# Kernel tuning notes

Hardware: AMD Instinct MI355X
Metric: run time of the kernel (lower is better)

## Reference

```python
import jax, jax.numpy as jnp
import numpy as np

B, NUM_CAMS, C, N_ANCHOR = 1, 6, 256, 900
NUM_LEVELS, NUM_FIXED, NUM_LEARN, NUM_GROUPS = 4, 7, 6, 8
NUM_PTS = NUM_FIXED + NUM_LEARN
IMG_W, IMG_H = 704, 256
SHAPES = [(64, 176), (32, 88), (16, 44), (8, 22)]  # strides 4,8,16,32


def setup_inputs() -> dict:
    key = jax.random.key(0)
    ks = jax.random.split(key, 12)
    sum_hw = sum(h * w for h, w in SHAPES)
    feature = jax.random.normal(ks[0], (B, NUM_CAMS, sum_hw, C), jnp.float32)
    spatial_shapes = jnp.array(SHAPES, dtype=jnp.int32)
    starts = np.cumsum([0] + [h * w for h, w in SHAPES[:-1]])
    level_start_index = jnp.array(starts, dtype=jnp.int32)
    # anchor: [x,y,z, log(w),log(l),log(h), sin(yaw), cos(yaw), vx,vy,vz]
    center = jax.random.uniform(ks[1], (B, N_ANCHOR, 3), minval=-40.0, maxval=40.0) * jnp.array([1.0, 1.0, 0.05])
    size = jnp.log(jnp.array([2.0, 4.5, 1.7])) * jnp.ones((B, N_ANCHOR, 3))
    yaw = jax.random.uniform(ks[2], (B, N_ANCHOR, 1), minval=-np.pi, maxval=np.pi)
    anchor = jnp.concatenate([center, size, jnp.sin(yaw), jnp.cos(yaw), jnp.zeros((B, N_ANCHOR, 3))], axis=-1).astype(jnp.float32)
    instance_feature = jax.random.normal(ks[3], (B, N_ANCHOR, C), jnp.float32)
    time_interval = jnp.full((B,), 0.5, jnp.float32)
    # plausible lidar2img = K @ [R|t] for 6 surround cameras
    l2i = []
    for c in range(NUM_CAMS):
        a = 2.0 * np.pi * c / NUM_CAMS
        Rz = np.array([[np.cos(a), -np.sin(a), 0.0], [np.sin(a), np.cos(a), 0.0], [0.0, 0.0, 1.0]])
        swap = np.array([[0.0, -1.0, 0.0], [0.0, 0.0, -1.0], [1.0, 0.0, 0.0]])  # lidar axes -> camera axes
        Rcam = swap @ Rz.T
        t = -Rcam @ np.array([0.0, 0.0, 1.5])
        E = np.eye(4); E[:3, :3] = Rcam; E[:3, 3] = t
        K = np.eye(4); K[0, 0] = K[1, 1] = 400.0; K[0, 2] = IMG_W / 2.0; K[1, 2] = IMG_H / 2.0
        l2i.append(K @ E)
    lidar2img = jnp.asarray(np.broadcast_to(np.stack(l2i)[None], (B, NUM_CAMS, 4, 4)), jnp.float32)
    image_wh = jnp.broadcast_to(jnp.array([IMG_W, IMG_H], jnp.float32), (B, NUM_CAMS, 2))
    s = 0.02
    n_w = NUM_CAMS * NUM_LEVELS * NUM_PTS * NUM_GROUPS
    return dict(
        instance_feature=instance_feature, anchor=anchor, time_interval=time_interval,
        feature=feature, spatial_shapes=spatial_shapes, level_start_index=level_start_index,
        lidar2img=lidar2img, image_wh=image_wh,
        enc_w=jax.random.normal(ks[4], (11, C)) * s, enc_b=jnp.zeros((C,), jnp.float32),
        kp_fixed=jax.random.normal(ks[5], (NUM_FIXED, 3)) * 0.5,
        kp_w=jax.random.normal(ks[6], (C, NUM_LEARN * 3)) * s, kp_b=jnp.zeros((NUM_LEARN * 3,), jnp.float32),
        wfc_w=jax.random.normal(ks[7], (C, n_w)) * s, wfc_b=jnp.zeros((n_w,), jnp.float32),
        out_w=jax.random.normal(ks[8], (C, C)) * s, out_b=jnp.zeros((C,), jnp.float32),
    )


def _bilinear_sample(feature, spatial_shapes, level_start_index, pts, valid):
    # feature: [B,Cm,sumHW,C]; pts: [B,Cm,N,P,2] normalized to [0,1]; valid: [B,Cm,N,P]
    Bn, Cm, _, Cd = feature.shape
    N, P = pts.shape[2], pts.shape[3]
    per_level = []
    for l in range(NUM_LEVELS):
        H = spatial_shapes[l, 0]
        W = spatial_shapes[l, 1]
        start = level_start_index[l]
        # grid_sample align_corners=False convention
        x = pts[..., 0] * W - 0.5
        y = pts[..., 1] * H - 0.5
        x0f = jnp.floor(x); y0f = jnp.floor(y)
        wx = (x - x0f)[..., None]
        wy = (y - y0f)[..., None]
        x0 = x0f.astype(jnp.int32); y0 = y0f.astype(jnp.int32)

        def gather(xi, yi):
            ok = (xi >= 0) & (xi < W) & (yi >= 0) & (yi < H) & valid
            xi_c = jnp.clip(xi, 0, W - 1)
            yi_c = jnp.clip(yi, 0, H - 1)
            idx = (start + yi_c * W + xi_c).reshape(Bn, Cm, N * P, 1)
            g = jnp.take_along_axis(feature, idx, axis=2).reshape(Bn, Cm, N, P, Cd)
            return g * ok[..., None]

        v = (gather(x0, y0) * (1 - wx) * (1 - wy)
             + gather(x0 + 1, y0) * wx * (1 - wy)
             + gather(x0, y0 + 1) * (1 - wx) * wy
             + gather(x0 + 1, y0 + 1) * wx * wy)
        per_level.append(v)
    return jnp.stack(per_level, axis=4)  # [B,Cm,N,P,L,C]


def _forward(instance_feature, anchor, feature, spatial_shapes, level_start_index,
             lidar2img, image_wh, enc_w, enc_b, kp_fixed, kp_w, kp_b, wfc_w, wfc_b, out_w, out_b):
    Bn, N, Cd = instance_feature.shape
    anchor_embed = anchor @ enc_w + enc_b                      # anchor_encoder
    # --- keypoint generation (7 fixed + 6 learnable), scaled by box size, rotated by yaw ---
    center = anchor[..., :3]
    size = jnp.exp(anchor[..., 3:6])
    sin_y, cos_y = anchor[..., 6:7], anchor[..., 7:8]
    learn = (instance_feature @ kp_w + kp_b).reshape(Bn, N, NUM_LEARN, 3)
    offs = jnp.concatenate([jnp.broadcast_to(kp_fixed, (Bn, N, NUM_FIXED, 3)), learn], axis=2)
    offs = offs * size[:, :, None, :]
    ox, oy, oz = offs[..., 0], offs[..., 1], offs[..., 2]
    rx = cos_y * ox - sin_y * oy
    ry = sin_y * ox + cos_y * oy
    kp = jnp.stack([rx, ry, oz], axis=-1) + center[:, :, None, :]          # [B,N,P,3]
    # --- project to each camera ---
    kp_h = jnp.concatenate([kp, jnp.ones_like(kp[..., :1])], axis=-1)
    p = jnp.einsum('bcij,bnpj->bcnpi', lidar2img, kp_h)                    # [B,Cm,N,P,4]
    depth = p[..., 2]
    xy = p[..., :2] / jnp.clip(depth, 1e-5, None)[..., None]
    pts = xy / image_wh[:, :, None, None, :]                               # [0,1] normalized
    valid = depth > 1e-5
    # --- multi-scale multi-camera bilinear gather ---
    feats = _bilinear_sample(feature, spatial_shapes, level_start_index, pts, valid)  # [B,Cm,N,P,L,C]
    # --- group-wise attention weights, softmax over cams*levels*pts ---
    w = ((instance_feature + anchor_embed) @ wfc_w + wfc_b).reshape(Bn, N, -1, NUM_GROUPS)
    w = jax.nn.softmax(w, axis=-2).reshape(Bn, N, NUM_CAMS, NUM_LEVELS, NUM_PTS, NUM_GROUPS)
    f = jnp.transpose(feats, (0, 2, 1, 4, 3, 5)).reshape(
        Bn, N, NUM_CAMS, NUM_LEVELS, NUM_PTS, NUM_GROUPS, Cd // NUM_GROUPS)
    agg = jnp.sum(f * w[..., None], axis=(2, 3, 4)).reshape(Bn, N, Cd)
    return instance_feature + (agg @ out_w + out_b)


def reference(instance_feature, anchor, time_interval, feature, spatial_shapes, level_start_index,
              lidar2img, image_wh, enc_w, enc_b, kp_fixed, kp_w, kp_b, wfc_w, wfc_b, out_w, out_b):
    # time_interval is only consumed by the 'refine' op, which is not in the executed op list
    return _forward(instance_feature, anchor, feature, spatial_shapes, level_start_index,
                    lidar2img, image_wh, enc_w, enc_b, kp_fixed, kp_w, kp_b, wfc_w, wfc_b, out_w, out_b)
```

## Files before the change

### kernel.cpp

```cpp
#include <hip/hip_runtime.h>
#include <math.h>

#define N_ANCHOR   900
#define NUM_CAMS   6
#define CDIM       256
#define NUM_LEVELS 4
#define NUM_FIXED  7
#define NUM_LEARN  6
#define NUM_PTS    13
#define NUM_GROUPS 8
#define NW         2496
#define NI         312
#define SUM_HW     14960

typedef short short8 __attribute__((ext_vector_type(8)));
typedef float floatx4 __attribute__((ext_vector_type(4)));

__device__ __forceinline__ unsigned short f2bf(float x) {
  unsigned u = __float_as_uint(x);
  u += 0x7FFFu + ((u >> 16) & 1u);
  return (unsigned short)(u >> 16);
}

__global__ __launch_bounds__(256) void k_prep(
    const float* __restrict__ inst, const float* __restrict__ anchor,
    const float* __restrict__ l2i, const float* __restrict__ image_wh,
    const float* __restrict__ kp_fixed, const float* __restrict__ kp_w,
    const float* __restrict__ kp_b,
    const float* __restrict__ enc_w, const float* __restrict__ enc_b,
    unsigned short* __restrict__ qbf, float* __restrict__ pts_out,
    float* __restrict__ valid_out) {
  const int n = blockIdx.x;
  const int t = threadIdx.x;
  __shared__ float anc[11];
  __shared__ float learn[NUM_LEARN * 3];
  __shared__ float kps[NUM_PTS][3];
  __shared__ float ins[CDIM];

  const float iv = inst[n * CDIM + t];
  ins[t] = iv;
  if (t < 11) anc[t] = anchor[n * 11 + t];
  __syncthreads();

  {
    float s = enc_b[t] + iv;
    #pragma unroll
    for (int k = 0; k < 11; ++k) s += anc[k] * enc_w[k * CDIM + t];
    qbf[n * CDIM + t] = f2bf(s);
  }

  if (t < NUM_LEARN * 3) {
    float s = kp_b[t];
    for (int k = 0; k < CDIM; ++k) s += ins[k] * kp_w[k * (NUM_LEARN * 3) + t];
    learn[t] = s;
  }
  __syncthreads();

  if (t < NUM_PTS) {
    const float sx = expf(anc[3]), sy = expf(anc[4]), sz = expf(anc[5]);
    float ox, oy, oz;
    if (t < NUM_FIXED) {
      ox = kp_fixed[t * 3 + 0]; oy = kp_fixed[t * 3 + 1]; oz = kp_fixed[t * 3 + 2];
    } else {
      const int j = (t - NUM_FIXED) * 3;
      ox = learn[j + 0]; oy = learn[j + 1]; oz = learn[j + 2];
    }
    ox *= sx; oy *= sy; oz *= sz;
    const float sn = anc[6], cs = anc[7];
    kps[t][0] = cs * ox - sn * oy + anc[0];
    kps[t][1] = sn * ox + cs * oy + anc[1];
    kps[t][2] = oz + anc[2];
  }
  __syncthreads();

  if (t < NUM_CAMS * NUM_PTS) {
    const int cam = t / NUM_PTS, p = t % NUM_PTS;
    const float* M = l2i + cam * 16;
    const float kx = kps[p][0], ky = kps[p][1], kz = kps[p][2];
    const float px = M[0] * kx + M[1] * ky + M[2]  * kz + M[3];
    const float py = M[4] * kx + M[5] * ky + M[6]  * kz + M[7];
    const float pz = M[8] * kx + M[9] * ky + M[10] * kz + M[11];
    const float d = fmaxf(pz, 1e-5f);
    const float u = (px / d) / image_wh[cam * 2 + 0];
    const float v = (py / d) / image_wh[cam * 2 + 1];
    const int o = n * NUM_CAMS * NUM_PTS + t;
    pts_out[o * 2 + 0] = u;
    pts_out[o * 2 + 1] = v;
    valid_out[o] = (pz > 1e-5f) ? 1.0f : 0.0f;
  }
}

__global__ __launch_bounds__(256) void k_cvtw(
    const float* __restrict__ wfc_w, unsigned short* __restrict__ wbf_t) {
  const int n0 = blockIdx.x * 64, k0 = blockIdx.y * 64;
  const int t = threadIdx.x;
  __shared__ float tile[64][65];
  #pragma unroll
  for (int i = 0; i < 4; ++i) {
    const int kr = (t >> 4) + i * 16;
    const int nc = (t & 15) * 4;
    const float4 v = *(const float4*)&wfc_w[(size_t)(k0 + kr) * NW + n0 + nc];
    tile[kr][nc + 0] = v.x; tile[kr][nc + 1] = v.y;
    tile[kr][nc + 2] = v.z; tile[kr][nc + 3] = v.w;
  }
  __syncthreads();
  #pragma unroll
  for (int i = 0; i < 4; ++i) {
    const int nr = (t >> 4) + i * 16;
    const int kc = (t & 15) * 4;
    ushort4 o;
    o.x = f2bf(tile[kc + 0][nr]);
    o.y = f2bf(tile[kc + 1][nr]);
    o.z = f2bf(tile[kc + 2][nr]);
    o.w = f2bf(tile[kc + 3][nr]);
    *(ushort4*)&wbf_t[(size_t)(n0 + nr) * CDIM + k0 + kc] = o;
  }
}

__global__ __launch_bounds__(256) void k_wgemm(
    const unsigned short* __restrict__ qbf,
    const unsigned short* __restrict__ wbf_t,
    const float* __restrict__ wfc_b, float* __restrict__ raw) {
  const int tid = threadIdx.x;
  const int w = tid >> 6;
  const int l = tid & 63;
  const int n0 = blockIdx.x * 64;
  const int m0 = blockIdx.y * 64;
  __shared__ unsigned short Bs[64 * 64];

  floatx4 acc[4];
  #pragma unroll
  for (int s = 0; s < 4; ++s) acc[s] = (floatx4){0.f, 0.f, 0.f, 0.f};

  const int arow = m0 + w * 16 + (l & 15);
  const bool arow_ok = arow < N_ANCHOR;
  const unsigned short* aptr = qbf + (size_t)arow * CDIM + (l >> 4) * 8;

  for (int k0 = 0; k0 < CDIM; k0 += 64) {
    #pragma unroll
    for (int i = 0; i < 2; ++i) {
      const int idx = tid + i * 256;
      const int n = idx >> 3, kg = idx & 7;
      const short8 bv =
          *(const short8*)&wbf_t[(size_t)(n0 + n) * CDIM + k0 + kg * 8];
      *(short8*)&Bs[n * 64 + ((kg ^ (n & 7)) * 8)] = bv;
    }
    __syncthreads();
    #pragma unroll
    for (int c = 0; c < 2; ++c) {
      short8 a = (short8){0, 0, 0, 0, 0, 0, 0, 0};
      if (arow_ok) a = *(const short8*)&aptr[k0 + c * 32];
      #pragma unroll
      for (int s = 0; s < 4; ++s) {
        const int nloc = s * 16 + (l & 15);
        const int k8 = c * 4 + (l >> 4);
        const short8 b = *(const short8*)&Bs[nloc * 64 + ((k8 ^ (nloc & 7)) * 8)];
        acc[s] = __builtin_amdgcn_mfma_f32_16x16x32_bf16(a, b, acc[s], 0, 0, 0);
      }
    }
    __syncthreads();
  }

  const int colb = n0 + (l & 15);
  const int rowb = m0 + w * 16 + (l >> 4) * 4;
  #pragma unroll
  for (int s = 0; s < 4; ++s) {
    const int col = colb + s * 16;
    const float bias = wfc_b[col];
    #pragma unroll
    for (int r = 0; r < 4; ++r) {
      const int row = rowb + r;
      if (row < N_ANCHOR)
        raw[(size_t)row * NW + col] = acc[s][r] + bias;
    }
  }
}

__global__ __launch_bounds__(256) void k_smstats(
    const float* __restrict__ raw, float* __restrict__ stats) {
  const int n = blockIdx.x, t = threadIdx.x;
  __shared__ float row_s[NW];
  const float4* src = (const float4*)(raw + (size_t)n * NW);
  for (int j = t; j < NW / 4; j += 256)
    *(float4*)&row_s[j * 4] = src[j];
  __syncthreads();
  const int g = t >> 5, lane = t & 31;
  float m = -1e30f;
  for (int i = lane; i < NI; i += 32) m = fmaxf(m, row_s[i * NUM_GROUPS + g]);
  #pragma unroll
  for (int o = 16; o > 0; o >>= 1) m = fmaxf(m, __shfl_down(m, o, 32));
  m = __shfl(m, 0, 32);
  float s = 0.0f;
  for (int i = lane; i < NI; i += 32) s += expf(row_s[i * NUM_GROUPS + g] - m);
  #pragma unroll
  for (int o = 16; o > 0; o >>= 1) s += __shfl_down(s, o, 32);
  if (lane == 0) {
    stats[n * 16 + g] = m;
    stats[n * 16 + 8 + g] = 1.0f / s;
  }
}

__global__ __launch_bounds__(256) void k_sample(
    const float* __restrict__ feature,
    const int* __restrict__ spatial_shapes, const int* __restrict__ level_start,
    const float* __restrict__ pts, const float* __restrict__ valid,
    const float* __restrict__ raw, const float* __restrict__ stats,
    float* __restrict__ agg) {
  const int n = blockIdx.x;
  const int cam = blockIdx.y;
  const int t = threadIdx.x;
  const int q = t >> 6;
  const int ci = t & 63;
  const int g = ci >> 3;
  __shared__ float w_s[NUM_LEVELS * NUM_PTS * NUM_GROUPS];
  __shared__ float uv_s[NUM_PTS][2];
  __shared__ float val_s[NUM_PTS];
  __shared__ float mx_s[NUM_GROUPS], inv_s[NUM_GROUPS];
  __shared__ int shp[NUM_LEVELS][2];
  __shared__ int lst[NUM_LEVELS];
  __shared__ int any_valid;
  __shared__ float4 red[256];

  if (t < NUM_PTS) {
    const int o = (n * NUM_CAMS + cam) * NUM_PTS + t;
    uv_s[t][0] = pts[o * 2 + 0];
    uv_s[t][1] = pts[o * 2 + 1];
    val_s[t] = valid[o];
  }
  if (t < NUM_GROUPS) {
    mx_s[t]  = stats[n * 16 + t];
    inv_s[t] = stats[n * 16 + 8 + t];
  }
  if (t < NUM_LEVELS) {
    shp[t][0] = spatial_shapes[t * 2 + 0];
    shp[t][1] = spatial_shapes[t * 2 + 1];
    lst[t] = level_start[t];
  }
  if (t == 0) any_valid = 0;
  __syncthreads();
  if (t < NUM_PTS && val_s[t] != 0.0f) any_valid = 1;
  __syncthreads();

  float* aout = agg + ((size_t)n * NUM_CAMS + cam) * CDIM;
  if (!any_valid) {
    if (t < 64) *(float4*)&aout[t * 4] = make_float4(0.f, 0.f, 0.f, 0.f);
    return;
  }

  for (int j = t; j < 416; j += 256)
    w_s[j] = expf(raw[(size_t)n * NW + cam * 416 + j] - mx_s[j & 7]) * inv_s[j & 7];
  __syncthreads();

  const int dx = q & 1, dy = q >> 1;
  float4 acc = make_float4(0.f, 0.f, 0.f, 0.f);
  const float* fcam = feature + (size_t)cam * SUM_HW * CDIM;
  for (int p = 0; p < NUM_PTS; ++p) {
    if (val_s[p] == 0.0f) continue;
    const float u = uv_s[p][0], v = uv_s[p][1];
    #pragma unroll
    for (int l = 0; l < NUM_LEVELS; ++l) {
      const int H = shp[l][0], W = shp[l][1], st = lst[l];
      const float x = u * (float)W - 0.5f;
      const float y = v * (float)H - 0.5f;
      const float x0f = floorf(x), y0f = floorf(y);
      const float wx = x - x0f, wy = y - y0f;
      const int xx = (int)x0f + dx;
      const int yy = (int)y0f + dy;
      if (xx >= 0 && xx < W && yy >= 0 && yy < H) {
        const float cw = w_s[(l * NUM_PTS + p) * 8 + g]
                       * (dx ? wx : 1.0f - wx) * (dy ? wy : 1.0f - wy);
        const float4 f = *(const float4*)&fcam[(size_t)(st + yy * W + xx) * CDIM + ci * 4];
        acc.x += cw * f.x; acc.y += cw * f.y;
        acc.z += cw * f.z; acc.w += cw * f.w;
      }
    }
  }
  red[t] = acc;
  __syncthreads();
  if (t < 64) {
    float4 s = red[t];
    const float4 b1 = red[t + 64], b2 = red[t + 128], b3 = red[t + 192];
    s.x += b1.x + b2.x + b3.x;
    s.y += b1.y + b2.y + b3.y;
    s.z += b1.z + b2.z + b3.z;
    s.w += b1.w + b2.w + b3.w;
    *(float4*)&aout[t * 4] = s;
  }
}

__global__ __launch_bounds__(1024) void k_out(
    const float* __restrict__ inst, const float* __restrict__ agg,
    const float* __restrict__ out_w, const float* __restrict__ out_b,
    float* __restrict__ out) {
  const int n = blockIdx.x, t = threadIdx.x;
  const int col = t & 255, ks = t >> 8;
  __shared__ float a_s[CDIM];
  __shared__ float red[4][CDIM];

  if (t < CDIM) {
    float s = 0.0f;
    #pragma unroll
    for (int cam = 0; cam < NUM_CAMS; ++cam)
      s += agg[((size_t)n * NUM_CAMS + cam) * CDIM + t];
    a_s[t] = s;
  }
  __syncthreads();

  float partial = 0.0f;
  const int k0 = ks * 64;
  #pragma unroll
  for (int k = 0; k < 64; ++k)
    partial += a_s[k0 + k] * out_w[(k0 + k) * CDIM + col];
  red[ks][col] = partial;
  __syncthreads();

  if (t < CDIM) {
    const float s = red[0][t] + red[1][t] + red[2][t] + red[3][t];
    out[(size_t)n * CDIM + t] = s + out_b[t] + inst[(size_t)n * CDIM + t];
  }
}

extern "C" void kernel_launch(void* const* d_in, const int* in_sizes, int n_in,
                              void* d_out, int out_size, void* d_ws, size_t ws_size,
                              hipStream_t stream) {
  const float* inst           = (const float*)d_in[0];
  const float* anchor         = (const float*)d_in[1];
  const float* feature        = (const float*)d_in[3];
  const int*   spatial_shapes = (const int*)d_in[4];
  const int*   level_start    = (const int*)d_in[5];
  const float* l2i            = (const float*)d_in[6];
  const float* image_wh       = (const float*)d_in[7];
  const float* enc_w          = (const float*)d_in[8];
  const float* enc_b          = (const float*)d_in[9];
  const float* kp_fixed       = (const float*)d_in[10];
  const float* kp_w           = (const float*)d_in[11];
  const float* kp_b           = (const float*)d_in[12];
  const float* wfc_w          = (const float*)d_in[13];
  const float* wfc_b          = (const float*)d_in[14];
  const float* out_w          = (const float*)d_in[15];
  const float* out_b          = (const float*)d_in[16];

  float* ws    = (float*)d_ws;
  float* pts   = ws;
  float* valid = pts + N_ANCHOR * NUM_CAMS * NUM_PTS * 2;
  float* wbuf  = valid + N_ANCHOR * NUM_CAMS * NUM_PTS;
  float* stats = wbuf + (size_t)N_ANCHOR * NW;
  float* agg   = stats + N_ANCHOR * 16;
  unsigned short* qbf   = (unsigned short*)(agg + N_ANCHOR * NUM_CAMS * CDIM);
  unsigned short* wbf_t = qbf + N_ANCHOR * CDIM;

  k_prep<<<N_ANCHOR, 256, 0, stream>>>(inst, anchor, l2i, image_wh,
                                       kp_fixed, kp_w, kp_b, enc_w, enc_b,
                                       qbf, pts, valid);
  k_cvtw<<<dim3(NW / 64, CDIM / 64), 256, 0, stream>>>(wfc_w, wbf_t);
  k_wgemm<<<dim3(NW / 64, (N_ANCHOR + 63) / 64), 256, 0, stream>>>(
      qbf, wbf_t, wfc_b, wbuf);
  k_smstats<<<N_ANCHOR, 256, 0, stream>>>(wbuf, stats);
  k_sample<<<dim3(N_ANCHOR, NUM_CAMS), 256, 0, stream>>>(
      feature, spatial_shapes, level_start, pts, valid, wbuf, stats, agg);
  k_out<<<N_ANCHOR, 1024, 0, stream>>>(inst, agg, out_w, out_b, (float*)d_out);
}
```

Before: 233.1 us.

## Compact valid sample taps via ballot and batch output GEMM over two anchors

In the sampling kernel, each wave now computes all 52 point-level tap offsets and bilinear coefficients in parallel. It compacts the in-bounds taps with a ballot/popcount into shared lists and then runs a branch-free loop unrolled by four over them. This removes per-tap divergent bounds checks and lets several independent feature loads be in flight at once. The output projection kernel now handles two anchors per block so each out_w load is reused twice, which halves weight traffic and the block count.

```diff
diff --git a/kernel.cpp b/kernel.cpp
--- a/kernel.cpp
+++ b/kernel.cpp
@@ -210,8 +210,8 @@
   const int cam = blockIdx.y;
   const int t = threadIdx.x;
   const int q = t >> 6;
-  const int ci = t & 63;
-  const int g = ci >> 3;
+  const int lane = t & 63;
+  const int g = lane >> 3;
   __shared__ float w_s[NUM_LEVELS * NUM_PTS * NUM_GROUPS];
   __shared__ float uv_s[NUM_PTS][2];
   __shared__ float val_s[NUM_PTS];
@@ -219,6 +219,9 @@
   __shared__ int shp[NUM_LEVELS][2];
   __shared__ int lst[NUM_LEVELS];
   __shared__ int any_valid;
+  __shared__ int   joff[4][56];
+  __shared__ float jcf[4][56];
+  __shared__ int   jw[4][56];
   __shared__ float4 red[256];
 
   if (t < NUM_PTS) {
@@ -249,30 +252,54 @@
 
   for (int j = t; j < 416; j += 256)
     w_s[j] = expf(raw[(size_t)n * NW + cam * 416 + j] - mx_s[j & 7]) * inv_s[j & 7];
-  __syncthreads();
-
-  const int dx = q & 1, dy = q >> 1;
-  float4 acc = make_float4(0.f, 0.f, 0.f, 0.f);
-  const float* fcam = feature + (size_t)cam * SUM_HW * CDIM;
-  for (int p = 0; p < NUM_PTS; ++p) {
-    if (val_s[p] == 0.0f) continue;
-    const float u = uv_s[p][0], v = uv_s[p][1];
-    #pragma unroll
-    for (int l = 0; l < NUM_LEVELS; ++l) {
+
+  bool ok = false;
+  int off = 0, wb = 0;
+  float cf = 0.0f;
+  if (lane < 52) {
+    const int p = lane >> 2, l = lane & 3;
+    if (val_s[p] != 0.0f) {
       const int H = shp[l][0], W = shp[l][1], st = lst[l];
-      const float x = u * (float)W - 0.5f;
-      const float y = v * (float)H - 0.5f;
+      const float x = uv_s[p][0] * (float)W - 0.5f;
+      const float y = uv_s[p][1] * (float)H - 0.5f;
       const float x0f = floorf(x), y0f = floorf(y);
       const float wx = x - x0f, wy = y - y0f;
+      const int dx = q & 1, dy = q >> 1;
       const int xx = (int)x0f + dx;
       const int yy = (int)y0f + dy;
       if (xx >= 0 && xx < W && yy >= 0 && yy < H) {
-        const float cw = w_s[(l * NUM_PTS + p) * 8 + g]
-                       * (dx ? wx : 1.0f - wx) * (dy ? wy : 1.0f - wy);
-        const float4 f = *(const float4*)&fcam[(size_t)(st + yy * W + xx) * CDIM + ci * 4];
-        acc.x += cw * f.x; acc.y += cw * f.y;
-        acc.z += cw * f.z; acc.w += cw * f.w;
+        ok = true;
+        off = (st + yy * W + xx) * CDIM;
+        cf = (dx ? wx : 1.0f - wx) * (dy ? wy : 1.0f - wy);
+        wb = (l * NUM_PTS + p) * 8;
       }
+    }
+  }
+  const unsigned long long mask = __ballot(ok);
+  const int nj = __popcll(mask);
+  if (ok) {
+    const int pos = __popcll(mask & ((1ull << lane) - 1ull));
+    joff[q][pos] = off;
+    jcf[q][pos] = cf;
+    jw[q][pos] = wb;
+  }
+  const int padded = (nj + 3) & ~3;
+  if (lane >= nj && lane < padded) {
+    joff[q][lane] = 0; jcf[q][lane] = 0.0f; jw[q][lane] = 0;
+  }
+  __syncthreads();
+
+  float4 acc = make_float4(0.f, 0.f, 0.f, 0.f);
+  const float* fcam = feature + (size_t)cam * SUM_HW * CDIM;
+  const int cio = lane * 4;
+  for (int j = 0; j < padded; j += 4) {
+    #pragma unroll
+    for (int i = 0; i < 4; ++i) {
+      const int o = joff[q][j + i];
+      const float wgt = jcf[q][j + i] * w_s[jw[q][j + i] + g];
+      const float4 f = *(const float4*)&fcam[o + cio];
+      acc.x += wgt * f.x; acc.y += wgt * f.y;
+      acc.z += wgt * f.z; acc.w += wgt * f.w;
     }
   }
   red[t] = acc;
@@ -292,31 +319,37 @@
     const float* __restrict__ inst, const float* __restrict__ agg,
     const float* __restrict__ out_w, const float* __restrict__ out_b,
     float* __restrict__ out) {
-  const int n = blockIdx.x, t = threadIdx.x;
+  const int n0 = blockIdx.x * 2, t = threadIdx.x;
   const int col = t & 255, ks = t >> 8;
-  __shared__ float a_s[CDIM];
-  __shared__ float red[4][CDIM];
-
-  if (t < CDIM) {
+  __shared__ float a_s[2][CDIM];
+  __shared__ float red[4][2][CDIM];
+
+  if (t < 512) {
+    const int a = t >> 8, c = t & 255;
     float s = 0.0f;
     #pragma unroll
     for (int cam = 0; cam < NUM_CAMS; ++cam)
-      s += agg[((size_t)n * NUM_CAMS + cam) * CDIM + t];
-    a_s[t] = s;
-  }
-  __syncthreads();
-
-  float partial = 0.0f;
+      s += agg[((size_t)(n0 + a) * NUM_CAMS + cam) * CDIM + c];
+    a_s[a][c] = s;
+  }
+  __syncthreads();
+
+  float p0 = 0.0f, p1 = 0.0f;
   const int k0 = ks * 64;
   #pragma unroll
-  for (int k = 0; k < 64; ++k)
-    partial += a_s[k0 + k] * out_w[(k0 + k) * CDIM + col];
-  red[ks][col] = partial;
-  __syncthreads();
-
-  if (t < CDIM) {
-    const float s = red[0][t] + red[1][t] + red[2][t] + red[3][t];
-    out[(size_t)n * CDIM + t] = s + out_b[t] + inst[(size_t)n * CDIM + t];
+  for (int k = 0; k < 64; ++k) {
+    const float w = out_w[(k0 + k) * CDIM + col];
+    p0 += a_s[0][k0 + k] * w;
+    p1 += a_s[1][k0 + k] * w;
+  }
+  red[ks][0][col] = p0;
+  red[ks][1][col] = p1;
+  __syncthreads();
+
+  if (t < 512) {
+    const int a = t >> 8, c = t & 255;
+    const float s = red[0][a][c] + red[1][a][c] + red[2][a][c] + red[3][a][c];
+    out[(size_t)(n0 + a) * CDIM + c] = s + out_b[c] + inst[(size_t)(n0 + a) * CDIM + c];
   }
 }
 
@@ -358,5 +391,5 @@
   k_smstats<<<N_ANCHOR, 256, 0, stream>>>(wbuf, stats);
   k_sample<<<dim3(N_ANCHOR, NUM_CAMS), 256, 0, stream>>>(
       feature, spatial_shapes, level_start, pts, valid, wbuf, stats, agg);
-  k_out<<<N_ANCHOR, 1024, 0, stream>>>(inst, agg, out_w, out_b, (float*)d_out);
-}
+  k_out<<<N_ANCHOR / 2, 1024, 0, stream>>>(inst, agg, out_w, out_b, (float*)d_out);
+}
```

Measured after the change: 213.9 us. 1.09x faster.

## Fuse softmax stats, sampling and output projection into one per-anchor kernel

Applied to the files above, without the earlier changes.

Merges the weight-conversion kernel into the prep kernel as extra blocks, and splits the keypoint linear layer across 144 threads with a partial-sum reduction. Softmax statistics, bilinear sampling across all cameras, and the output projection now run in a single 1024-thread block per anchor. That block builds a compacted job list of in-bounds bilinear taps with a shared atomic counter and spreads the jobs across 16 waves. This removes three launches, the stats and agg round-trips through global memory, and the idle lanes left by invalid points, at the cost of large per-block shared memory and lower occupancy.

```diff
diff --git a/kernel.cpp b/kernel.cpp
--- a/kernel.cpp
+++ b/kernel.cpp
@@ -12,6 +12,7 @@
 #define NW         2496
 #define NI         312
 #define SUM_HW     14960
+#define MAXJOBS    1248
 
 typedef short short8 __attribute__((ext_vector_type(8)));
 typedef float floatx4 __attribute__((ext_vector_type(4)));
@@ -22,18 +23,48 @@
   return (unsigned short)(u >> 16);
 }
 
-__global__ __launch_bounds__(256) void k_prep(
+__global__ __launch_bounds__(256) void k_pre(
     const float* __restrict__ inst, const float* __restrict__ anchor,
     const float* __restrict__ l2i, const float* __restrict__ image_wh,
     const float* __restrict__ kp_fixed, const float* __restrict__ kp_w,
     const float* __restrict__ kp_b,
     const float* __restrict__ enc_w, const float* __restrict__ enc_b,
-    unsigned short* __restrict__ qbf, float* __restrict__ pts_out,
-    float* __restrict__ valid_out) {
+    const float* __restrict__ wfc_w,
+    unsigned short* __restrict__ qbf, unsigned short* __restrict__ wbf_t,
+    float* __restrict__ pts_out, float* __restrict__ valid_out) {
+  const int t = threadIdx.x;
+
+  if (blockIdx.x >= N_ANCHOR) {
+    const int bi = blockIdx.x - N_ANCHOR;
+    const int n0 = (bi % 39) * 64, k0 = (bi / 39) * 64;
+    __shared__ float tile[64][65];
+    #pragma unroll
+    for (int i = 0; i < 4; ++i) {
+      const int kr = (t >> 4) + i * 16;
+      const int nc = (t & 15) * 4;
+      const float4 v = *(const float4*)&wfc_w[(size_t)(k0 + kr) * NW + n0 + nc];
+      tile[kr][nc + 0] = v.x; tile[kr][nc + 1] = v.y;
+      tile[kr][nc + 2] = v.z; tile[kr][nc + 3] = v.w;
+    }
+    __syncthreads();
+    #pragma unroll
+    for (int i = 0; i < 4; ++i) {
+      const int nr = (t >> 4) + i * 16;
+      const int kc = (t & 15) * 4;
+      ushort4 o;
+      o.x = f2bf(tile[kc + 0][nr]);
+      o.y = f2bf(tile[kc + 1][nr]);
+      o.z = f2bf(tile[kc + 2][nr]);
+      o.w = f2bf(tile[kc + 3][nr]);
+      *(ushort4*)&wbf_t[(size_t)(n0 + nr) * CDIM + k0 + kc] = o;
+    }
+    return;
+  }
+
   const int n = blockIdx.x;
-  const int t = threadIdx.x;
   __shared__ float anc[11];
   __shared__ float learn[NUM_LEARN * 3];
+  __shared__ float psum[8][NUM_LEARN * 3];
   __shared__ float kps[NUM_PTS][3];
   __shared__ float ins[CDIM];
 
@@ -49,9 +80,20 @@
     qbf[n * CDIM + t] = f2bf(s);
   }
 
+  if (t < 144) {
+    const int c = t / 18, j = t % 18;
+    float s = 0.0f;
+    const int k0 = c * 32;
+    #pragma unroll
+    for (int k = 0; k < 32; ++k)
+      s += ins[k0 + k] * kp_w[(k0 + k) * (NUM_LEARN * 3) + j];
+    psum[c][j] = s;
+  }
+  __syncthreads();
   if (t < NUM_LEARN * 3) {
     float s = kp_b[t];
-    for (int k = 0; k < CDIM; ++k) s += ins[k] * kp_w[k * (NUM_LEARN * 3) + t];
+    #pragma unroll
+    for (int c = 0; c < 8; ++c) s += psum[c][t];
     learn[t] = s;
   }
   __syncthreads();
@@ -90,33 +132,6 @@
   }
 }
 
-__global__ __launch_bounds__(256) void k_cvtw(
-    const float* __restrict__ wfc_w, unsigned short* __restrict__ wbf_t) {
-  const int n0 = blockIdx.x * 64, k0 = blockIdx.y * 64;
-  const int t = threadIdx.x;
-  __shared__ float tile[64][65];
-  #pragma unroll
-  for (int i = 0; i < 4; ++i) {
-    const int kr = (t >> 4) + i * 16;
-    const int nc = (t & 15) * 4;
-    const float4 v = *(const float4*)&wfc_w[(size_t)(k0 + kr) * NW + n0 + nc];
-    tile[kr][nc + 0] = v.x; tile[kr][nc + 1] = v.y;
-    tile[kr][nc + 2] = v.z; tile[kr][nc + 3] = v.w;
-  }
-  __syncthreads();
-  #pragma unroll
-  for (int i = 0; i < 4; ++i) {
-    const int nr = (t >> 4) + i * 16;
-    const int kc = (t & 15) * 4;
-    ushort4 o;
-    o.x = f2bf(tile[kc + 0][nr]);
-    o.y = f2bf(tile[kc + 1][nr]);
-    o.z = f2bf(tile[kc + 2][nr]);
-    o.w = f2bf(tile[kc + 3][nr]);
-    *(ushort4*)&wbf_t[(size_t)(n0 + nr) * CDIM + k0 + kc] = o;
-  }
-}
-
 __global__ __launch_bounds__(256) void k_wgemm(
     const unsigned short* __restrict__ qbf,
     const unsigned short* __restrict__ wbf_t,
@@ -176,146 +191,141 @@
   }
 }
 
-__global__ __launch_bounds__(256) void k_smstats(
-    const float* __restrict__ raw, float* __restrict__ stats) {
-  const int n = blockIdx.x, t = threadIdx.x;
-  __shared__ float row_s[NW];
-  const float4* src = (const float4*)(raw + (size_t)n * NW);
-  for (int j = t; j < NW / 4; j += 256)
-    *(float4*)&row_s[j * 4] = src[j];
-  __syncthreads();
-  const int g = t >> 5, lane = t & 31;
-  float m = -1e30f;
-  for (int i = lane; i < NI; i += 32) m = fmaxf(m, row_s[i * NUM_GROUPS + g]);
-  #pragma unroll
-  for (int o = 16; o > 0; o >>= 1) m = fmaxf(m, __shfl_down(m, o, 32));
-  m = __shfl(m, 0, 32);
-  float s = 0.0f;
-  for (int i = lane; i < NI; i += 32) s += expf(row_s[i * NUM_GROUPS + g] - m);
-  #pragma unroll
-  for (int o = 16; o > 0; o >>= 1) s += __shfl_down(s, o, 32);
-  if (lane == 0) {
-    stats[n * 16 + g] = m;
-    stats[n * 16 + 8 + g] = 1.0f / s;
-  }
-}
-
-__global__ __launch_bounds__(256) void k_sample(
+__global__ __launch_bounds__(1024) void k_mega(
     const float* __restrict__ feature,
     const int* __restrict__ spatial_shapes, const int* __restrict__ level_start,
     const float* __restrict__ pts, const float* __restrict__ valid,
-    const float* __restrict__ raw, const float* __restrict__ stats,
-    float* __restrict__ agg) {
+    const float* __restrict__ raw,
+    const float* __restrict__ inst,
+    const float* __restrict__ out_w, const float* __restrict__ out_b,
+    float* __restrict__ out) {
   const int n = blockIdx.x;
-  const int cam = blockIdx.y;
   const int t = threadIdx.x;
-  const int q = t >> 6;
-  const int ci = t & 63;
-  const int g = ci >> 3;
-  __shared__ float w_s[NUM_LEVELS * NUM_PTS * NUM_GROUPS];
-  __shared__ float uv_s[NUM_PTS][2];
-  __shared__ float val_s[NUM_PTS];
+  const int wv = t >> 6;
+  const int lane = t & 63;
+  const int g = lane >> 3;
+
+  __shared__ float w_row[NW];
+  __shared__ float uv_s[NUM_CAMS * NUM_PTS][2];
+  __shared__ float val_s[NUM_CAMS * NUM_PTS];
   __shared__ float mx_s[NUM_GROUPS], inv_s[NUM_GROUPS];
   __shared__ int shp[NUM_LEVELS][2];
   __shared__ int lst[NUM_LEVELS];
-  __shared__ int any_valid;
-  __shared__ float4 red[256];
-
-  if (t < NUM_PTS) {
-    const int o = (n * NUM_CAMS + cam) * NUM_PTS + t;
+  __shared__ int joff[MAXJOBS];
+  __shared__ float jcf[MAXJOBS];
+  __shared__ int jw_s[MAXJOBS];
+  __shared__ int njobs;
+  __shared__ float4 red4[16][64];
+  __shared__ float a_s[CDIM];
+  __shared__ float red2[4][CDIM];
+
+  {
+    const float4* src = (const float4*)(raw + (size_t)n * NW);
+    for (int j = t; j < NW / 4; j += 1024) *(float4*)&w_row[j * 4] = src[j];
+  }
+  if (t < NUM_CAMS * NUM_PTS) {
+    const int o = n * NUM_CAMS * NUM_PTS + t;
     uv_s[t][0] = pts[o * 2 + 0];
     uv_s[t][1] = pts[o * 2 + 1];
     val_s[t] = valid[o];
-  }
-  if (t < NUM_GROUPS) {
-    mx_s[t]  = stats[n * 16 + t];
-    inv_s[t] = stats[n * 16 + 8 + t];
   }
   if (t < NUM_LEVELS) {
     shp[t][0] = spatial_shapes[t * 2 + 0];
     shp[t][1] = spatial_shapes[t * 2 + 1];
     lst[t] = level_start[t];
   }
-  if (t == 0) any_valid = 0;
-  __syncthreads();
-  if (t < NUM_PTS && val_s[t] != 0.0f) any_valid = 1;
-  __syncthreads();
-
-  float* aout = agg + ((size_t)n * NUM_CAMS + cam) * CDIM;
-  if (!any_valid) {
-    if (t < 64) *(float4*)&aout[t * 4] = make_float4(0.f, 0.f, 0.f, 0.f);
-    return;
-  }
-
-  for (int j = t; j < 416; j += 256)
-    w_s[j] = expf(raw[(size_t)n * NW + cam * 416 + j] - mx_s[j & 7]) * inv_s[j & 7];
-  __syncthreads();
-
-  const int dx = q & 1, dy = q >> 1;
-  float4 acc = make_float4(0.f, 0.f, 0.f, 0.f);
-  const float* fcam = feature + (size_t)cam * SUM_HW * CDIM;
-  for (int p = 0; p < NUM_PTS; ++p) {
-    if (val_s[p] == 0.0f) continue;
-    const float u = uv_s[p][0], v = uv_s[p][1];
-    #pragma unroll
-    for (int l = 0; l < NUM_LEVELS; ++l) {
+  if (t == 0) njobs = 0;
+  __syncthreads();
+
+  if (t < 256) {
+    const int sg = t >> 5, sl = t & 31;
+    float m = -1e30f;
+    for (int i = sl; i < NI; i += 32) m = fmaxf(m, w_row[i * NUM_GROUPS + sg]);
+    #pragma unroll
+    for (int o = 16; o > 0; o >>= 1) m = fmaxf(m, __shfl_down(m, o, 32));
+    m = __shfl(m, 0, 32);
+    float s = 0.0f;
+    for (int i = sl; i < NI; i += 32) s += expf(w_row[i * NUM_GROUPS + sg] - m);
+    #pragma unroll
+    for (int o = 16; o > 0; o >>= 1) s += __shfl_down(s, o, 32);
+    if (sl == 0) { mx_s[sg] = m; inv_s[sg] = 1.0f / s; }
+  }
+
+  for (int jt = t; jt < MAXJOBS; jt += 1024) {
+    const int cam = jt / 208;
+    const int r = jt % 208;
+    const int q = r / 52;
+    const int pl = r % 52;
+    const int p = pl >> 2, l = pl & 3;
+    if (val_s[cam * NUM_PTS + p] != 0.0f) {
       const int H = shp[l][0], W = shp[l][1], st = lst[l];
-      const float x = u * (float)W - 0.5f;
-      const float y = v * (float)H - 0.5f;
+      const float x = uv_s[cam * NUM_PTS + p][0] * (float)W - 0.5f;
+      const float y = uv_s[cam * NUM_PTS + p][1] * (float)H - 0.5f;
       const float x0f = floorf(x), y0f = floorf(y);
       const float wx = x - x0f, wy = y - y0f;
+      const int dx = q & 1, dy = q >> 1;
       const int xx = (int)x0f + dx;
       const int yy = (int)y0f + dy;
       if (xx >= 0 && xx < W && yy >= 0 && yy < H) {
-        const float cw = w_s[(l * NUM_PTS + p) * 8 + g]
-                       * (dx ? wx : 1.0f - wx) * (dy ? wy : 1.0f - wy);
-        const float4 f = *(const float4*)&fcam[(size_t)(st + yy * W + xx) * CDIM + ci * 4];
-        acc.x += cw * f.x; acc.y += cw * f.y;
-        acc.z += cw * f.z; acc.w += cw * f.w;
+        const int pos = atomicAdd(&njobs, 1);
+        joff[pos] = (cam * SUM_HW + st + yy * W + xx) * CDIM;
+        jcf[pos] = (dx ? wx : 1.0f - wx) * (dy ? wy : 1.0f - wy);
+        jw_s[pos] = (cam * 52 + l * NUM_PTS + p) * 8;
       }
     }
   }
-  red[t] = acc;
-  __syncthreads();
+  __syncthreads();
+
+  const int nj = njobs;
+  const int padded = (nj + 31) & ~31;
+  for (int j = nj + t; j < padded; j += 1024) {
+    joff[j] = 0; jcf[j] = 0.0f; jw_s[j] = 0;
+  }
+  for (int j = t; j < NW; j += 1024)
+    w_row[j] = expf(w_row[j] - mx_s[j & 7]) * inv_s[j & 7];
+  __syncthreads();
+
+  float4 acc = make_float4(0.f, 0.f, 0.f, 0.f);
+  const int cio = lane * 4;
+  for (int j = wv; j < padded; j += 32) {
+    const int o0 = joff[j];
+    const float wg0 = jcf[j] * w_row[jw_s[j] + g];
+    const float4 f0 = *(const float4*)&feature[o0 + cio];
+    const int j1 = j + 16;
+    const int o1 = joff[j1];
+    const float wg1 = jcf[j1] * w_row[jw_s[j1] + g];
+    const float4 f1 = *(const float4*)&feature[o1 + cio];
+    acc.x += wg0 * f0.x + wg1 * f1.x;
+    acc.y += wg0 * f0.y + wg1 * f1.y;
+    acc.z += wg0 * f0.z + wg1 * f1.z;
+    acc.w += wg0 * f0.w + wg1 * f1.w;
+  }
+  red4[wv][lane] = acc;
+  __syncthreads();
+
   if (t < 64) {
-    float4 s = red[t];
-    const float4 b1 = red[t + 64], b2 = red[t + 128], b3 = red[t + 192];
-    s.x += b1.x + b2.x + b3.x;
-    s.y += b1.y + b2.y + b3.y;
-    s.z += b1.z + b2.z + b3.z;
-    s.w += b1.w + b2.w + b3.w;
-    *(float4*)&aout[t * 4] = s;
-  }
-}
-
-__global__ __launch_bounds__(1024) void k_out(
-    const float* __restrict__ inst, const float* __restrict__ agg,
-    const float* __restrict__ out_w, const float* __restrict__ out_b,
-    float* __restrict__ out) {
-  const int n = blockIdx.x, t = threadIdx.x;
-  const int col = t & 255, ks = t >> 8;
-  __shared__ float a_s[CDIM];
-  __shared__ float red[4][CDIM];
-
+    float4 s = red4[0][t];
+    #pragma unroll
+    for (int w = 1; w < 16; ++w) {
+      const float4 b = red4[w][t];
+      s.x += b.x; s.y += b.y; s.z += b.z; s.w += b.w;
+    }
+    *(float4*)&a_s[t * 4] = s;
+  }
+  __syncthreads();
+
+  {
+    const int col = t & 255, ks = t >> 8;
+    float p = 0.0f;
+    const int k0 = ks * 64;
+    #pragma unroll
+    for (int k = 0; k < 64; ++k)
+      p += a_s[k0 + k] * out_w[(k0 + k) * CDIM + col];
+    red2[ks][col] = p;
+  }
+  __syncthreads();
   if (t < CDIM) {
-    float s = 0.0f;
-    #pragma unroll
-    for (int cam = 0; cam < NUM_CAMS; ++cam)
-      s += agg[((size_t)n * NUM_CAMS + cam) * CDIM + t];
-    a_s[t] = s;
-  }
-  __syncthreads();
-
-  float partial = 0.0f;
-  const int k0 = ks * 64;
-  #pragma unroll
-  for (int k = 0; k < 64; ++k)
-    partial += a_s[k0 + k] * out_w[(k0 + k) * CDIM + col];
-  red[ks][col] = partial;
-  __syncthreads();
-
-  if (t < CDIM) {
-    const float s = red[0][t] + red[1][t] + red[2][t] + red[3][t];
+    const float s = red2[0][t] + red2[1][t] + red2[2][t] + red2[3][t];
     out[(size_t)n * CDIM + t] = s + out_b[t] + inst[(size_t)n * CDIM + t];
   }
 }
@@ -344,19 +354,15 @@
   float* pts   = ws;
   float* valid = pts + N_ANCHOR * NUM_CAMS * NUM_PTS * 2;
   float* wbuf  = valid + N_ANCHOR * NUM_CAMS * NUM_PTS;
-  float* stats = wbuf + (size_t)N_ANCHOR * NW;
-  float* agg   = stats + N_ANCHOR * 16;
-  unsigned short* qbf   = (unsigned short*)(agg + N_ANCHOR * NUM_CAMS * CDIM);
+  unsigned short* qbf   = (unsigned short*)(wbuf + (size_t)N_ANCHOR * NW);
   unsigned short* wbf_t = qbf + N_ANCHOR * CDIM;
 
-  k_prep<<<N_ANCHOR, 256, 0, stream>>>(inst, anchor, l2i, image_wh,
-                                       kp_fixed, kp_w, kp_b, enc_w, enc_b,
-                                       qbf, pts, valid);
-  k_cvtw<<<dim3(NW / 64, CDIM / 64), 256, 0, stream>>>(wfc_w, wbf_t);
+  k_pre<<<N_ANCHOR + 156, 256, 0, stream>>>(
+      inst, anchor, l2i, image_wh, kp_fixed, kp_w, kp_b, enc_w, enc_b,
+      wfc_w, qbf, wbf_t, pts, valid);
   k_wgemm<<<dim3(NW / 64, (N_ANCHOR + 63) / 64), 256, 0, stream>>>(
       qbf, wbf_t, wfc_b, wbuf);
-  k_smstats<<<N_ANCHOR, 256, 0, stream>>>(wbuf, stats);
-  k_sample<<<dim3(N_ANCHOR, NUM_CAMS), 256, 0, stream>>>(
-      feature, spatial_shapes, level_start, pts, valid, wbuf, stats, agg);
-  k_out<<<N_ANCHOR, 1024, 0, stream>>>(inst, agg, out_w, out_b, (float*)d_out);
-}
+  k_mega<<<N_ANCHOR, 1024, 0, stream>>>(
+      feature, spatial_shapes, level_start, pts, valid, wbuf,
+      inst, out_w, out_b, (float*)d_out);
+}
```

Result: faster. 209.6 us (-10.1%).
